# Kernel tuning notes

Hardware: AMD Instinct MI355X
Metric: run time of the kernel (lower is better)

The kernel has to match this reference:

```python
import jax, jax.numpy as jnp
import numpy as np

N_NODES = 100000
N_EDGES = 1600000
NFEAT, NHID, NCLASS = 256, 128, 40
N_CROSS = 20000


def setup_inputs() -> dict:
    key = jax.random.key(0)
    ks = jax.random.split(key, 16)
    s = 0.05
    return {
        "x": jax.random.normal(ks[0], (N_NODES, NFEAT), dtype=jnp.float32),
        "W0": jax.random.normal(ks[1], (NFEAT, NHID), dtype=jnp.float32) * s,
        "b0": jnp.zeros((NHID,), dtype=jnp.float32),
        "W1": jax.random.normal(ks[2], (NHID, NHID), dtype=jnp.float32) * s,
        "b1": jnp.zeros((NHID,), dtype=jnp.float32),
        "W2": jax.random.normal(ks[3], (NHID, NCLASS), dtype=jnp.float32) * s,
        "b2": jnp.zeros((NCLASS,), dtype=jnp.float32),
        "hist0": jax.random.normal(ks[4], (N_NODES, NHID), dtype=jnp.float32),
        "hist1": jax.random.normal(ks[5], (N_NODES, NHID), dtype=jnp.float32),
        "edge_src": jax.random.randint(ks[6], (N_EDGES,), 0, N_NODES, dtype=jnp.int32),
        "edge_dst": jax.random.randint(ks[7], (N_EDGES,), 0, N_NODES, dtype=jnp.int32),
        "idx_data0": jax.random.randint(ks[8], (N_CROSS,), 0, N_NODES, dtype=jnp.int32),
        "idx_com0": jax.random.randint(ks[9], (N_CROSS,), 0, N_NODES, dtype=jnp.int32),
        "idx_data1": jax.random.randint(ks[10], (N_CROSS,), 0, N_NODES, dtype=jnp.int32),
        "idx_com1": jax.random.randint(ks[11], (N_CROSS,), 0, N_NODES, dtype=jnp.int32),
    }


def reference(x, W0, b0, W1, b1, W2, b2, hist0, hist1,
              edge_src, edge_dst, idx_data0, idx_com0, idx_data1, idx_com1):
    N = x.shape[0]
    # GCN normalization with self-loops: A_hat = D^-1/2 (A + I) D^-1/2
    loops = jnp.arange(N, dtype=edge_src.dtype)
    src = jnp.concatenate([edge_src, loops])
    dst = jnp.concatenate([edge_dst, loops])
    deg = jax.ops.segment_sum(jnp.ones_like(dst, dtype=x.dtype), dst, num_segments=N)
    dis = jax.lax.rsqrt(jnp.maximum(deg, 1.0))  # deg >= 1 due to self-loops
    norm = (dis[src] * dis[dst])[:, None]       # [E+N, 1]

    def conv(h, W, b):
        h = h @ W                                             # [N, out]
        msg = h[src] * norm                                   # [E+N, out]
        return jax.ops.segment_sum(msg, dst, num_segments=N) + b

    # layer 0 + history overwrite (dropout is identity in eval mode)
    h = jax.nn.relu(conv(x, W0, b0))
    h = h.at[idx_com0].set(hist0[idx_data0])
    # layer 1 + history overwrite
    h = jax.nn.relu(conv(h, W1, b1))
    h = h.at[idx_com1].set(hist1[idx_data1])
    # final layer + log_softmax
    out = conv(h, W2, b2)
    return jax.nn.log_softmax(out, axis=-1)
```

## Files before the change

### kernel.cpp

```cpp
#include <hip/hip_runtime.h>
#include <cmath>

#define NFEAT 256
#define NHID  128
#define NCLASS 40
#define MAXNB 800
#define CHUNK 8192


__global__ __launch_bounds__(256)
void P1_hist(const int* __restrict__ dst, int* __restrict__ bh, int E, int NB){
  __shared__ int lh[MAXNB];
  for(int t = threadIdx.x; t < NB; t += 256) lh[t] = 0;
  __syncthreads();
  for(int i = blockIdx.x*256 + threadIdx.x; i < E; i += gridDim.x*256)
    atomicAdd(&lh[dst[i] >> 7], 1);
  __syncthreads();
  for(int t = threadIdx.x; t < NB; t += 256){
    int c = lh[t];
    if(c) atomicAdd(&bh[t], c);
  }
}

__global__ __launch_bounds__(1024)
void P2_scan(const int* __restrict__ bh, int* __restrict__ boff, int* __restrict__ bcur,
             int* __restrict__ off, int N, int E, int NB){
  __shared__ int sc[1024];
  int t = threadIdx.x;
  int v = (t < NB) ? bh[t] : 0;
  sc[t] = v; __syncthreads();
  for(int o = 1; o < 1024; o <<= 1){
    int a = sc[t] + ((t >= o) ? sc[t-o] : 0);
    __syncthreads();
    sc[t] = a;
    __syncthreads();
  }
  int ex = sc[t] - v;
  if(t < NB){ boff[t] = ex; bcur[t] = ex; }
  if(t == 0){ boff[NB] = E; off[N] = E; }
}

__global__ __launch_bounds__(256)
void P3_part(const int* __restrict__ src, const int* __restrict__ dst,
             int* __restrict__ bcur, int2* __restrict__ tmp, int E, int NB){
  __shared__ int dstS[CHUNK];
  __shared__ int lh[MAXNB];
  __shared__ int lcur[MAXNB];
  int base = blockIdx.x * CHUNK;
  int n = E - base; if(n > CHUNK) n = CHUNK;
  for(int t = threadIdx.x; t < NB; t += 256){ lh[t] = 0; lcur[t] = 0; }
  __syncthreads();
  for(int j = threadIdx.x; j < n; j += 256){
    int d = dst[base + j];
    dstS[j] = d;
    atomicAdd(&lh[d >> 7], 1);
  }
  __syncthreads();
  for(int t = threadIdx.x; t < NB; t += 256){
    int c = lh[t];
    if(c) lh[t] = atomicAdd(&bcur[t], c);
  }
  __syncthreads();
  for(int j = threadIdx.x; j < n; j += 256){
    int d = dstS[j];
    int b = d >> 7;
    int p = lh[b] + atomicAdd(&lcur[b], 1);
    tmp[p] = make_int2(src[base + j], d);
  }
}

__global__ __launch_bounds__(256)
void P4_build(const int2* __restrict__ tmp, const int* __restrict__ boff,
              int* __restrict__ off, float* __restrict__ dis,
              int* __restrict__ csr, int N){
  __shared__ int2 eS[3072];
  __shared__ int cnt[128], sc[128], cur[128];
  int b = blockIdx.x;
  int s = boff[b], e = boff[b+1];
  int ne = e - s;
  int n0 = b * 128;
  if(threadIdx.x < 128){ cnt[threadIdx.x] = 0; cur[threadIdx.x] = 0; }
  __syncthreads();
  bool fits = (ne <= 3072);
  for(int i = threadIdx.x; i < ne; i += 256){
    int2 p = tmp[s + i];
    if(fits) eS[i] = p;
    atomicAdd(&cnt[p.y & 127], 1);
  }
  __syncthreads();
  if(threadIdx.x < 128) sc[threadIdx.x] = cnt[threadIdx.x];
  __syncthreads();
  for(int o = 1; o < 128; o <<= 1){
    int a = 0;
    if(threadIdx.x < 128) a = sc[threadIdx.x] + ((threadIdx.x >= o) ? sc[threadIdx.x - o] : 0);
    __syncthreads();
    if(threadIdx.x < 128) sc[threadIdx.x] = a;
    __syncthreads();
  }
  if(threadIdx.x < 128){
    int node = n0 + threadIdx.x;
    if(node < N){
      int c = cnt[threadIdx.x];
      off[node] = s + sc[threadIdx.x] - c;
      dis[node] = rsqrtf((float)(c + 1));
    }
  }
  __syncthreads();
  for(int i = threadIdx.x; i < ne; i += 256){
    int2 p = fits ? eS[i] : tmp[s + i];
    int l = p.y & 127;
    int pos = s + (sc[l] - cnt[l]) + atomicAdd(&cur[l], 1);
    csr[pos] = p.x;
  }
}


template<int K, int NOUT>
__global__ __launch_bounds__(256)
void gemm_scale(const float* __restrict__ A, const float* __restrict__ W,
                const float* __restrict__ dis, float* __restrict__ C, int M)
{
  constexpr int BM = 128, BN = 64, BK = 16;
  __shared__ float As[BK][BM + 4];
  __shared__ float Ws[BK][BN];
  const int tid = threadIdx.x;
  const int tr = tid & 15;
  const int tc = tid >> 4;
  const int m0 = blockIdx.x * BM;
  const int n0 = blockIdx.y * BN;

  float acc[8][4];
  #pragma unroll
  for(int i = 0; i < 8; i++)
    #pragma unroll
    for(int j = 0; j < 4; j++) acc[i][j] = 0.f;

  for(int k0 = 0; k0 < K; k0 += BK){
    #pragma unroll
    for(int j = 0; j < 2; j++){
      int idx = tid + j*256;
      int row = idx & 127;
      int kq  = idx >> 7;
      float4 v = {0.f,0.f,0.f,0.f};
      int grow = m0 + row;
      if(grow < M) v = *reinterpret_cast<const float4*>(&A[(size_t)grow*K + k0 + kq*4]);
      As[kq*4+0][row] = v.x; As[kq*4+1][row] = v.y;
      As[kq*4+2][row] = v.z; As[kq*4+3][row] = v.w;
    }
    {
      int row = tid >> 4;
      int cq  = tid & 15;
      int col = n0 + cq*4;
      float4 v = {0.f,0.f,0.f,0.f};
      if(col + 3 < NOUT) v = *reinterpret_cast<const float4*>(&W[(size_t)(k0+row)*NOUT + col]);
      *reinterpret_cast<float4*>(&Ws[row][cq*4]) = v;
    }
    __syncthreads();
    #pragma unroll
    for(int k = 0; k < BK; k++){
      float4 a0 = *reinterpret_cast<const float4*>(&As[k][tr*8]);
      float4 a1 = *reinterpret_cast<const float4*>(&As[k][tr*8 + 4]);
      float4 bv = *reinterpret_cast<const float4*>(&Ws[k][tc*4]);
      float a[8] = {a0.x,a0.y,a0.z,a0.w,a1.x,a1.y,a1.z,a1.w};
      float bb[4] = {bv.x,bv.y,bv.z,bv.w};
      #pragma unroll
      for(int i = 0; i < 8; i++)
        #pragma unroll
        for(int j = 0; j < 4; j++)
          acc[i][j] += a[i]*bb[j];
    }
    __syncthreads();
  }
  #pragma unroll
  for(int i = 0; i < 8; i++){
    int grow = m0 + tr*8 + i;
    if(grow >= M) continue;
    int col = n0 + tc*4;
    if(col >= NOUT) continue;
    float d = dis[grow];
    float4 v;
    v.x = acc[i][0]*d; v.y = acc[i][1]*d; v.z = acc[i][2]*d; v.w = acc[i][3]*d;
    *reinterpret_cast<float4*>(&C[(size_t)grow*NOUT + col]) = v;
  }
}


__global__ __launch_bounds__(256)
void agg_relu128(const float* __restrict__ T, const int* __restrict__ off,
                 const int* __restrict__ csr, const float* __restrict__ dis,
                 const float* __restrict__ bias, float* __restrict__ H, int N)
{
  int node = blockIdx.x*4 + (threadIdx.x >> 6);
  if(node >= N) return;
  int lane = threadIdx.x & 63;
  int half = lane >> 5;
  int sl = lane & 31;
  int s = off[node], e = off[node+1];
  const float4* T4 = (const float4*)T;
  float4 acc = {0.f,0.f,0.f,0.f};
  for(int i = s + half; i < e; i += 2){
    int u = csr[i];
    float4 v = T4[(size_t)u*32 + sl];
    acc.x += v.x; acc.y += v.y; acc.z += v.z; acc.w += v.w;
  }
  if(half == 0){
    float4 v = T4[(size_t)node*32 + sl];
    acc.x += v.x; acc.y += v.y; acc.z += v.z; acc.w += v.w;
  }
  acc.x += __shfl_down(acc.x, 32, 64);
  acc.y += __shfl_down(acc.y, 32, 64);
  acc.z += __shfl_down(acc.z, 32, 64);
  acc.w += __shfl_down(acc.w, 32, 64);
  if(lane < 32){
    float di = dis[node];
    float4 b = ((const float4*)bias)[sl];
    float4 o;
    o.x = fmaxf(di*acc.x + b.x, 0.f);
    o.y = fmaxf(di*acc.y + b.y, 0.f);
    o.z = fmaxf(di*acc.z + b.z, 0.f);
    o.w = fmaxf(di*acc.w + b.w, 0.f);
    ((float4*)H)[(size_t)node*32 + sl] = o;
  }
}

__global__ __launch_bounds__(256)
void agg_softmax40(const float* __restrict__ T, const int* __restrict__ off,
                   const int* __restrict__ csr, const float* __restrict__ dis,
                   const float* __restrict__ bias, float* __restrict__ OUT, int N)
{
  int node = blockIdx.x*4 + (threadIdx.x >> 6);
  if(node >= N) return;
  int lane = threadIdx.x & 63;
  int g  = lane / 20;
  int sl = lane - g*20;
  int s = off[node], e = off[node+1];
  const float2* T2 = (const float2*)T;
  float ax = 0.f, ay = 0.f;
  if(g < 3){
    for(int i = s + g; i < e; i += 3){
      int u = csr[i];
      float2 v = T2[(size_t)u*20 + sl];
      ax += v.x; ay += v.y;
    }
    if(g == 0){
      float2 v = T2[(size_t)node*20 + sl];
      ax += v.x; ay += v.y;
    }
  }
  ax += __shfl(ax, lane + 20, 64) + __shfl(ax, lane + 40, 64);
  ay += __shfl(ay, lane + 20, 64) + __shfl(ay, lane + 40, 64);
  float di = dis[node];
  float vx = -1e30f, vy = -1e30f;
  if(lane < 20){
    float2 b = ((const float2*)bias)[sl];
    vx = di*ax + b.x;
    vy = di*ay + b.y;
  }
  float m = fmaxf(vx, vy);
  #pragma unroll
  for(int o = 1; o < 32; o <<= 1) m = fmaxf(m, __shfl_xor(m, o, 32));
  float ex = (lane < 20) ? (expf(vx - m) + expf(vy - m)) : 0.f;
  float ssum = ex;
  #pragma unroll
  for(int o = 1; o < 32; o <<= 1) ssum += __shfl_xor(ssum, o, 32);
  float lse = m + logf(ssum);
  if(lane < 20){
    float2 o2; o2.x = vx - lse; o2.y = vy - lse;
    ((float2*)OUT)[(size_t)node*20 + sl] = o2;
  }
}


__global__ void k_stamp(const int* __restrict__ idx_com, int* __restrict__ stamp, int n){
  int j = blockIdx.x*256 + threadIdx.x;
  if(j < n) atomicMax(&stamp[idx_com[j]], j);
}

__global__ __launch_bounds__(256)
void k_overwrite(const int* __restrict__ idx_com, const int* __restrict__ idx_data,
                 const int* __restrict__ stamp, const float* __restrict__ hist,
                 float* __restrict__ H, int n)
{
  int j = blockIdx.x*4 + (threadIdx.x >> 6);
  if(j >= n) return;
  int lane = threadIdx.x & 63;
  int c = idx_com[j];
  if(stamp[c] != j) return;
  int d = idx_data[j];
  ((float2*)H)[(size_t)c*64 + lane] = ((const float2*)hist)[(size_t)d*64 + lane];
}


extern "C" void kernel_launch(void* const* d_in, const int* in_sizes, int n_in,
                              void* d_out, int out_size, void* d_ws, size_t ws_size,
                              hipStream_t stream)
{
  const float* x     = (const float*)d_in[0];
  const float* W0    = (const float*)d_in[1];
  const float* b0    = (const float*)d_in[2];
  const float* W1    = (const float*)d_in[3];
  const float* b1    = (const float*)d_in[4];
  const float* W2    = (const float*)d_in[5];
  const float* b2    = (const float*)d_in[6];
  const float* hist0 = (const float*)d_in[7];
  const float* hist1 = (const float*)d_in[8];
  const int* esrc = (const int*)d_in[9];
  const int* edst = (const int*)d_in[10];
  const int* idx_data0 = (const int*)d_in[11];
  const int* idx_com0  = (const int*)d_in[12];
  const int* idx_data1 = (const int*)d_in[13];
  const int* idx_com1  = (const int*)d_in[14];

  const int N  = in_sizes[0] / NFEAT;
  const int E  = in_sizes[9];
  const int NC = in_sizes[11];
  const int NB = (N + 127) / 128;

  char* p = (char*)d_ws;
  auto carve = [&](size_t bytes) -> void* {
    void* r = (void*)p;
    p += (bytes + 255) & ~(size_t)255;
    return r;
  };
  int*   bh    = (int*)  carve((size_t)NB*4);
  int*   boff  = (int*)  carve((size_t)(NB+1)*4);
  int*   bcur  = (int*)  carve((size_t)NB*4);
  int*   off   = (int*)  carve((size_t)(N+1)*4);
  int*   stamp = (int*)  carve((size_t)N*4);
  int*   csr   = (int*)  carve((size_t)E*4);
  float* dis   = (float*)carve((size_t)N*4);
  float* bufA  = (float*)carve((size_t)N*NHID*4);
  float* bufB  = (float*)carve((size_t)N*NHID*4);
  size_t cbytes = (size_t)N*NCLASS*4;
  size_t tbytes = (size_t)E*8;
  float* bufC  = (float*)carve(cbytes > tbytes ? cbytes : tbytes);
  int2*  tmp   = (int2*)bufC;

  hipMemsetAsync(bh, 0, (size_t)NB*4, stream);
  P1_hist<<<256, 256, 0, stream>>>(edst, bh, E, NB);
  P2_scan<<<1, 1024, 0, stream>>>(bh, boff, bcur, off, N, E, NB);
  P3_part<<<(E + CHUNK - 1)/CHUNK, 256, 0, stream>>>(esrc, edst, bcur, tmp, E, NB);
  P4_build<<<NB, 256, 0, stream>>>(tmp, boff, off, dis, csr, N);

  dim3 g0((N + 127)/128, 2);
  gemm_scale<NFEAT, NHID><<<g0, 256, 0, stream>>>(x, W0, dis, bufA, N);
  agg_relu128<<<(N+3)/4, 256, 0, stream>>>(bufA, off, csr, dis, b0, bufB, N);

  hipMemsetAsync(stamp, 0xFF, (size_t)N*4, stream);
  k_stamp<<<(NC+255)/256, 256, 0, stream>>>(idx_com0, stamp, NC);
  k_overwrite<<<(NC+3)/4, 256, 0, stream>>>(idx_com0, idx_data0, stamp, hist0, bufB, NC);

  dim3 g1((N + 127)/128, 2);
  gemm_scale<NHID, NHID><<<g1, 256, 0, stream>>>(bufB, W1, dis, bufA, N);
  agg_relu128<<<(N+3)/4, 256, 0, stream>>>(bufA, off, csr, dis, b1, bufB, N);

  hipMemsetAsync(stamp, 0xFF, (size_t)N*4, stream);
  k_stamp<<<(NC+255)/256, 256, 0, stream>>>(idx_com1, stamp, NC);
  k_overwrite<<<(NC+3)/4, 256, 0, stream>>>(idx_com1, idx_data1, stamp, hist1, bufB, NC);

  dim3 g2((N + 127)/128, 1);
  gemm_scale<NHID, NCLASS><<<g2, 256, 0, stream>>>(bufB, W2, dis, bufC, N);
  agg_softmax40<<<(N+3)/4, 256, 0, stream>>>(bufC, off, csr, dis, b2, (float*)d_out, N);
}
```

Baseline: 797.8 us.

## Use full-width 128x128 GEMM tile and unroll gather loops with multiple accumulators

Adds a GEMM kernel that computes all 128 output columns per block with an 8x8 register tile per thread. This halves the number of times the A matrix is read compared with two 64-column blocks. The neighbour-aggregation loops in both aggregation kernels are unrolled with independent accumulators, so several gathers are in flight at once and memory latency is hidden. The cost is higher register pressure in the GEMM, which may reduce occupancy.

```diff
diff --git a/kernel.cpp b/kernel.cpp
--- a/kernel.cpp
+++ b/kernel.cpp
@@ -114,6 +114,75 @@
   }
 }
 
+
+template<int K>
+__global__ __launch_bounds__(256)
+void gemm128_scale(const float* __restrict__ A, const float* __restrict__ W,
+                   const float* __restrict__ dis, float* __restrict__ C, int M)
+{
+  constexpr int BM = 128, BK = 16;
+  __shared__ float As[BK][BM + 4];
+  __shared__ float Ws[BK][128 + 4];
+  const int tid = threadIdx.x;
+  const int tr = tid >> 4;
+  const int tc = tid & 15;
+  const int m0 = blockIdx.x * BM;
+
+  float acc[8][8];
+  #pragma unroll
+  for(int i = 0; i < 8; i++)
+    #pragma unroll
+    for(int j = 0; j < 8; j++) acc[i][j] = 0.f;
+
+  for(int k0 = 0; k0 < K; k0 += BK){
+    #pragma unroll
+    for(int j = 0; j < 2; j++){
+      int idx = tid + j*256;
+      int row = idx & 127;
+      int kq  = idx >> 7;
+      float4 v = {0.f,0.f,0.f,0.f};
+      int gr = m0 + row;
+      if(gr < M) v = *reinterpret_cast<const float4*>(&A[(size_t)gr*K + k0 + kq*4]);
+      As[kq*4+0][row] = v.x; As[kq*4+1][row] = v.y;
+      As[kq*4+2][row] = v.z; As[kq*4+3][row] = v.w;
+    }
+    #pragma unroll
+    for(int j = 0; j < 2; j++){
+      int idx = tid + j*256;
+      int row = idx >> 5;
+      int cq  = idx & 31;
+      float4 v = *reinterpret_cast<const float4*>(&W[(size_t)(k0+row)*128 + cq*4]);
+      *reinterpret_cast<float4*>(&Ws[row][cq*4]) = v;
+    }
+    __syncthreads();
+    #pragma unroll
+    for(int k = 0; k < BK; k++){
+      float4 a0 = *reinterpret_cast<const float4*>(&As[k][tr*4]);
+      float4 a1 = *reinterpret_cast<const float4*>(&As[k][64 + tr*4]);
+      float4 b0 = *reinterpret_cast<const float4*>(&Ws[k][tc*4]);
+      float4 b1 = *reinterpret_cast<const float4*>(&Ws[k][64 + tc*4]);
+      float a[8] = {a0.x,a0.y,a0.z,a0.w, a1.x,a1.y,a1.z,a1.w};
+      float b[8] = {b0.x,b0.y,b0.z,b0.w, b1.x,b1.y,b1.z,b1.w};
+      #pragma unroll
+      for(int i = 0; i < 8; i++)
+        #pragma unroll
+        for(int j = 0; j < 8; j++)
+          acc[i][j] += a[i]*b[j];
+    }
+    __syncthreads();
+  }
+  #pragma unroll
+  for(int i = 0; i < 8; i++){
+    int gr = m0 + ((i < 4) ? (tr*4 + i) : (64 + tr*4 + (i - 4)));
+    if(gr >= M) continue;
+    float d = dis[gr];
+    float4 v0, v1;
+    v0.x = acc[i][0]*d; v0.y = acc[i][1]*d; v0.z = acc[i][2]*d; v0.w = acc[i][3]*d;
+    v1.x = acc[i][4]*d; v1.y = acc[i][5]*d; v1.z = acc[i][6]*d; v1.w = acc[i][7]*d;
+    *reinterpret_cast<float4*>(&C[(size_t)gr*128 + tc*4]) = v0;
+    *reinterpret_cast<float4*>(&C[(size_t)gr*128 + 64 + tc*4]) = v1;
+  }
+}
 
 template<int K, int NOUT>
 __global__ __launch_bounds__(256)
@@ -197,16 +266,33 @@
   int sl = lane & 31;
   int s = off[node], e = off[node+1];
   const float4* T4 = (const float4*)T;
-  float4 acc = {0.f,0.f,0.f,0.f};
-  for(int i = s + half; i < e; i += 2){
+  float4 a0 = {0.f,0.f,0.f,0.f}, a1 = a0, a2 = a0, a3 = a0;
+  int i = s + half;
+  for(; i + 6 < e; i += 8){
+    int u0 = csr[i], u1 = csr[i+2], u2 = csr[i+4], u3 = csr[i+6];
+    float4 v0 = T4[(size_t)u0*32 + sl];
+    float4 v1 = T4[(size_t)u1*32 + sl];
+    float4 v2 = T4[(size_t)u2*32 + sl];
+    float4 v3 = T4[(size_t)u3*32 + sl];
+    a0.x += v0.x; a0.y += v0.y; a0.z += v0.z; a0.w += v0.w;
+    a1.x += v1.x; a1.y += v1.y; a1.z += v1.z; a1.w += v1.w;
+    a2.x += v2.x; a2.y += v2.y; a2.z += v2.z; a2.w += v2.w;
+    a3.x += v3.x; a3.y += v3.y; a3.z += v3.z; a3.w += v3.w;
+  }
+  for(; i < e; i += 2){
     int u = csr[i];
     float4 v = T4[(size_t)u*32 + sl];
-    acc.x += v.x; acc.y += v.y; acc.z += v.z; acc.w += v.w;
+    a0.x += v.x; a0.y += v.y; a0.z += v.z; a0.w += v.w;
   }
   if(half == 0){
     float4 v = T4[(size_t)node*32 + sl];
-    acc.x += v.x; acc.y += v.y; acc.z += v.z; acc.w += v.w;
-  }
+    a0.x += v.x; a0.y += v.y; a0.z += v.z; a0.w += v.w;
+  }
+  float4 acc;
+  acc.x = a0.x + a1.x + a2.x + a3.x;
+  acc.y = a0.y + a1.y + a2.y + a3.y;
+  acc.z = a0.z + a1.z + a2.z + a3.z;
+  acc.w = a0.w + a1.w + a2.w + a3.w;
   acc.x += __shfl_down(acc.x, 32, 64);
   acc.y += __shfl_down(acc.y, 32, 64);
   acc.z += __shfl_down(acc.z, 32, 64);
@@ -235,9 +321,19 @@
   int sl = lane - g*20;
   int s = off[node], e = off[node+1];
   const float2* T2 = (const float2*)T;
-  float ax = 0.f, ay = 0.f;
+  float ax = 0.f, ay = 0.f, bx = 0.f, by = 0.f, cx = 0.f, cy = 0.f;
   if(g < 3){
-    for(int i = s + g; i < e; i += 3){
+    int i = s + g;
+    for(; i + 6 < e; i += 9){
+      int u0 = csr[i], u1 = csr[i+3], u2 = csr[i+6];
+      float2 v0 = T2[(size_t)u0*20 + sl];
+      float2 v1 = T2[(size_t)u1*20 + sl];
+      float2 v2 = T2[(size_t)u2*20 + sl];
+      ax += v0.x; ay += v0.y;
+      bx += v1.x; by += v1.y;
+      cx += v2.x; cy += v2.y;
+    }
+    for(; i < e; i += 3){
       int u = csr[i];
       float2 v = T2[(size_t)u*20 + sl];
       ax += v.x; ay += v.y;
@@ -246,6 +342,7 @@
       float2 v = T2[(size_t)node*20 + sl];
       ax += v.x; ay += v.y;
     }
+    ax += bx + cx; ay += by + cy;
   }
   ax += __shfl(ax, lane + 20, 64) + __shfl(ax, lane + 40, 64);
   ay += __shfl(ay, lane + 20, 64) + __shfl(ay, lane + 40, 64);
@@ -342,23 +439,20 @@
   P3_part<<<(E + CHUNK - 1)/CHUNK, 256, 0, stream>>>(esrc, edst, bcur, tmp, E, NB);
   P4_build<<<NB, 256, 0, stream>>>(tmp, boff, off, dis, csr, N);
 
-  dim3 g0((N + 127)/128, 2);
-  gemm_scale<NFEAT, NHID><<<g0, 256, 0, stream>>>(x, W0, dis, bufA, N);
+  gemm128_scale<NFEAT><<<dim3((N + 127)/128, 1), 256, 0, stream>>>(x, W0, dis, bufA, N);
   agg_relu128<<<(N+3)/4, 256, 0, stream>>>(bufA, off, csr, dis, b0, bufB, N);
 
   hipMemsetAsync(stamp, 0xFF, (size_t)N*4, stream);
   k_stamp<<<(NC+255)/256, 256, 0, stream>>>(idx_com0, stamp, NC);
   k_overwrite<<<(NC+3)/4, 256, 0, stream>>>(idx_com0, idx_data0, stamp, hist0, bufB, NC);
 
-  dim3 g1((N + 127)/128, 2);
-  gemm_scale<NHID, NHID><<<g1, 256, 0, stream>>>(bufB, W1, dis, bufA, N);
+  gemm128_scale<NHID><<<dim3((N + 127)/128, 1), 256, 0, stream>>>(bufB, W1, dis, bufA, N);
   agg_relu128<<<(N+3)/4, 256, 0, stream>>>(bufA, off, csr, dis, b1, bufB, N);
 
   hipMemsetAsync(stamp, 0xFF, (size_t)N*4, stream);
   k_stamp<<<(NC+255)/256, 256, 0, stream>>>(idx_com1, stamp, NC);
   k_overwrite<<<(NC+3)/4, 256, 0, stream>>>(idx_com1, idx_data1, stamp, hist1, bufB, NC);
 
-  dim3 g2((N + 127)/128, 1);
-  gemm_scale<NHID, NCLASS><<<g2, 256, 0, stream>>>(bufB, W2, dis, bufC, N);
+  gemm_scale<NHID, NCLASS><<<dim3((N + 127)/128, 1), 256, 0, stream>>>(bufB, W2, dis, bufC, N);
   agg_softmax40<<<(N+3)/4, 256, 0, stream>>>(bufC, off, csr, dis, b2, (float*)d_out, N);
 }
```

Result: faster. 777.6 us (-2.5%).

## Use split-bf16 MFMA GEMMs and unroll neighbor aggregation loops

Applied to the files above, without the earlier changes.

Replaces the fp32 SIMT GEMMs with MFMA bf16 kernels. Each fp32 operand is split into high and low bf16 parts, and three MFMA products are summed to keep near-fp32 accuracy. Weights are pre-split and transposed by a small kernel on each call. The aggregation kernels also gain 4-way and 3-way unrolled gather loops with independent accumulators to expose more memory-level parallelism. This adds per-call weight-split launches and costs some precision versus true fp32.

```diff
diff --git a/kernel.cpp b/kernel.cpp
--- a/kernel.cpp
+++ b/kernel.cpp
@@ -6,6 +6,20 @@
 #define NCLASS 40
 #define MAXNB 800
 #define CHUNK 8192
+
+typedef __attribute__((ext_vector_type(8))) short bf16x8;
+typedef __attribute__((ext_vector_type(4))) float f32x4;
+
+__device__ __forceinline__ unsigned short f2bf(float f){
+  unsigned u = __float_as_uint(f);
+  u += 0x7FFFu + ((u >> 16) & 1u);
+  return (unsigned short)(u >> 16);
+}
+__device__ __forceinline__ void fsplit(float f, unsigned short &h, unsigned short &l){
+  h = f2bf(f);
+  float fh = __uint_as_float(((unsigned)h) << 16);
+  l = f2bf(f - fh);
+}
 
 
 __global__ __launch_bounds__(256)
@@ -115,72 +129,117 @@
 }
 
 
-template<int K, int NOUT>
-__global__ __launch_bounds__(256)
-void gemm_scale(const float* __restrict__ A, const float* __restrict__ W,
-                const float* __restrict__ dis, float* __restrict__ C, int M)
+__global__ void k_wsplit(const float* __restrict__ W, unsigned short* __restrict__ WTh,
+                         unsigned short* __restrict__ WTl, int K, int NOUT){
+  int n = blockIdx.x;
+  for(int k = threadIdx.x; k < K; k += blockDim.x){
+    float f = (n < NOUT) ? W[(size_t)k*NOUT + n] : 0.f;
+    unsigned short h, l;
+    fsplit(f, h, l);
+    WTh[(size_t)n*K + k] = h;
+    WTl[(size_t)n*K + k] = l;
+  }
+}
+
+
+template<int K, int BN>
+__global__ __launch_bounds__(256, 2)
+void gemm_mfma_scale(const float* __restrict__ A,
+                     const unsigned short* __restrict__ WTh,
+                     const unsigned short* __restrict__ WTl,
+                     const float* __restrict__ dis,
+                     float* __restrict__ C, int M, int NOUT)
 {
-  constexpr int BM = 128, BN = 64, BK = 16;
-  __shared__ float As[BK][BM + 4];
-  __shared__ float Ws[BK][BN];
-  const int tid = threadIdx.x;
-  const int tr = tid & 15;
-  const int tc = tid >> 4;
+  constexpr int BM = 128, BK = 32;
+  constexpr int WM = (BN == 128) ? 64 : 32;
+  constexpr int WN = 64;
+  constexpr int NWN = BN / WN;
+  constexpr int MF = WM / 16, NF = WN / 16;
+  __shared__ __align__(16) unsigned short AsH[BM][BK];
+  __shared__ __align__(16) unsigned short AsL[BM][BK];
+  __shared__ __align__(16) unsigned short WsH[BN][BK];
+  __shared__ __align__(16) unsigned short WsL[BN][BK];
+
+  const int tid  = threadIdx.x;
+  const int wave = tid >> 6;
+  const int lane = tid & 63;
+  const int wm = wave / NWN;
+  const int wn = wave % NWN;
   const int m0 = blockIdx.x * BM;
-  const int n0 = blockIdx.y * BN;
-
-  float acc[8][4];
+  const int lr = lane & 15;
+  const int lg = lane >> 4;
+
+  f32x4 acc[MF][NF];
   #pragma unroll
-  for(int i = 0; i < 8; i++)
-    #pragma unroll
-    for(int j = 0; j < 4; j++) acc[i][j] = 0.f;
+  for(int i = 0; i < MF; i++)
+    #pragma unroll
+    for(int j = 0; j < NF; j++)
+      acc[i][j] = (f32x4){0.f,0.f,0.f,0.f};
 
   for(int k0 = 0; k0 < K; k0 += BK){
     #pragma unroll
-    for(int j = 0; j < 2; j++){
-      int idx = tid + j*256;
-      int row = idx & 127;
-      int kq  = idx >> 7;
+    for(int j = 0; j < 4; j++){
+      int s   = tid + j*256;
+      int row = s >> 3;
+      int kq  = (s & 7) * 4;
       float4 v = {0.f,0.f,0.f,0.f};
-      int grow = m0 + row;
-      if(grow < M) v = *reinterpret_cast<const float4*>(&A[(size_t)grow*K + k0 + kq*4]);
-      As[kq*4+0][row] = v.x; As[kq*4+1][row] = v.y;
-      As[kq*4+2][row] = v.z; As[kq*4+3][row] = v.w;
-    }
-    {
-      int row = tid >> 4;
-      int cq  = tid & 15;
-      int col = n0 + cq*4;
-      float4 v = {0.f,0.f,0.f,0.f};
-      if(col + 3 < NOUT) v = *reinterpret_cast<const float4*>(&W[(size_t)(k0+row)*NOUT + col]);
-      *reinterpret_cast<float4*>(&Ws[row][cq*4]) = v;
-    }
-    __syncthreads();
-    #pragma unroll
-    for(int k = 0; k < BK; k++){
-      float4 a0 = *reinterpret_cast<const float4*>(&As[k][tr*8]);
-      float4 a1 = *reinterpret_cast<const float4*>(&As[k][tr*8 + 4]);
-      float4 bv = *reinterpret_cast<const float4*>(&Ws[k][tc*4]);
-      float a[8] = {a0.x,a0.y,a0.z,a0.w,a1.x,a1.y,a1.z,a1.w};
-      float bb[4] = {bv.x,bv.y,bv.z,bv.w};
+      if(m0 + row < M) v = *reinterpret_cast<const float4*>(&A[(size_t)(m0+row)*K + k0 + kq]);
+      ushort4 h, l;
+      fsplit(v.x, h.x, l.x); fsplit(v.y, h.y, l.y);
+      fsplit(v.z, h.z, l.z); fsplit(v.w, h.w, l.w);
+      *reinterpret_cast<ushort4*>(&AsH[row][kq]) = h;
+      *reinterpret_cast<ushort4*>(&AsL[row][kq]) = l;
+    }
+    constexpr int WSLOTS = BN * BK / 8;
+    #pragma unroll
+    for(int s = 0; s < WSLOTS; s += 256){
+      int ss = s + tid;
+      int n  = ss >> 2;
+      int kq = (ss & 3) * 8;
+      *reinterpret_cast<uint4*>(&WsH[n][kq]) =
+          *reinterpret_cast<const uint4*>(&WTh[(size_t)n*K + k0 + kq]);
+      *reinterpret_cast<uint4*>(&WsL[n][kq]) =
+          *reinterpret_cast<const uint4*>(&WTl[(size_t)n*K + k0 + kq]);
+    }
+    __syncthreads();
+
+    bf16x8 ah[MF], al[MF], bh[NF], bl[NF];
+    #pragma unroll
+    for(int i = 0; i < MF; i++){
+      ah[i] = *reinterpret_cast<const bf16x8*>(&AsH[wm*WM + i*16 + lr][lg*8]);
+      al[i] = *reinterpret_cast<const bf16x8*>(&AsL[wm*WM + i*16 + lr][lg*8]);
+    }
+    #pragma unroll
+    for(int j = 0; j < NF; j++){
+      bh[j] = *reinterpret_cast<const bf16x8*>(&WsH[wn*WN + j*16 + lr][lg*8]);
+      bl[j] = *reinterpret_cast<const bf16x8*>(&WsL[wn*WN + j*16 + lr][lg*8]);
+    }
+    #pragma unroll
+    for(int i = 0; i < MF; i++)
       #pragma unroll
-      for(int i = 0; i < 8; i++)
-        #pragma unroll
-        for(int j = 0; j < 4; j++)
-          acc[i][j] += a[i]*bb[j];
-    }
-    __syncthreads();
-  }
+      for(int j = 0; j < NF; j++){
+        acc[i][j] = __builtin_amdgcn_mfma_f32_16x16x32_bf16(ah[i], bh[j], acc[i][j], 0, 0, 0);
+        acc[i][j] = __builtin_amdgcn_mfma_f32_16x16x32_bf16(ah[i], bl[j], acc[i][j], 0, 0, 0);
+        acc[i][j] = __builtin_amdgcn_mfma_f32_16x16x32_bf16(al[i], bh[j], acc[i][j], 0, 0, 0);
+      }
+    __syncthreads();
+  }
+
   #pragma unroll
-  for(int i = 0; i < 8; i++){
-    int grow = m0 + tr*8 + i;
-    if(grow >= M) continue;
-    int col = n0 + tc*4;
-    if(col >= NOUT) continue;
-    float d = dis[grow];
-    float4 v;
-    v.x = acc[i][0]*d; v.y = acc[i][1]*d; v.z = acc[i][2]*d; v.w = acc[i][3]*d;
-    *reinterpret_cast<float4*>(&C[(size_t)grow*NOUT + col]) = v;
+  for(int i = 0; i < MF; i++){
+    int rbase = m0 + wm*WM + i*16 + lg*4;
+    #pragma unroll
+    for(int r = 0; r < 4; r++){
+      int row = rbase + r;
+      if(row >= M) continue;
+      float d = dis[row];
+      #pragma unroll
+      for(int j = 0; j < NF; j++){
+        int col = wn*WN + j*16 + lr;
+        if(col < NOUT)
+          C[(size_t)row*NOUT + col] = acc[i][j][r] * d;
+      }
+    }
   }
 }
 
@@ -197,16 +256,33 @@
   int sl = lane & 31;
   int s = off[node], e = off[node+1];
   const float4* T4 = (const float4*)T;
-  float4 acc = {0.f,0.f,0.f,0.f};
-  for(int i = s + half; i < e; i += 2){
+  float4 a0 = {0.f,0.f,0.f,0.f}, a1 = a0, a2 = a0, a3 = a0;
+  int i = s + half;
+  for(; i + 6 < e; i += 8){
+    int u0 = csr[i], u1 = csr[i+2], u2 = csr[i+4], u3 = csr[i+6];
+    float4 v0 = T4[(size_t)u0*32 + sl];
+    float4 v1 = T4[(size_t)u1*32 + sl];
+    float4 v2 = T4[(size_t)u2*32 + sl];
+    float4 v3 = T4[(size_t)u3*32 + sl];
+    a0.x += v0.x; a0.y += v0.y; a0.z += v0.z; a0.w += v0.w;
+    a1.x += v1.x; a1.y += v1.y; a1.z += v1.z; a1.w += v1.w;
+    a2.x += v2.x; a2.y += v2.y; a2.z += v2.z; a2.w += v2.w;
+    a3.x += v3.x; a3.y += v3.y; a3.z += v3.z; a3.w += v3.w;
+  }
+  for(; i < e; i += 2){
     int u = csr[i];
     float4 v = T4[(size_t)u*32 + sl];
-    acc.x += v.x; acc.y += v.y; acc.z += v.z; acc.w += v.w;
+    a0.x += v.x; a0.y += v.y; a0.z += v.z; a0.w += v.w;
   }
   if(half == 0){
     float4 v = T4[(size_t)node*32 + sl];
-    acc.x += v.x; acc.y += v.y; acc.z += v.z; acc.w += v.w;
-  }
+    a0.x += v.x; a0.y += v.y; a0.z += v.z; a0.w += v.w;
+  }
+  float4 acc;
+  acc.x = a0.x + a1.x + a2.x + a3.x;
+  acc.y = a0.y + a1.y + a2.y + a3.y;
+  acc.z = a0.z + a1.z + a2.z + a3.z;
+  acc.w = a0.w + a1.w + a2.w + a3.w;
   acc.x += __shfl_down(acc.x, 32, 64);
   acc.y += __shfl_down(acc.y, 32, 64);
   acc.z += __shfl_down(acc.z, 32, 64);
@@ -235,9 +311,19 @@
   int sl = lane - g*20;
   int s = off[node], e = off[node+1];
   const float2* T2 = (const float2*)T;
-  float ax = 0.f, ay = 0.f;
+  float ax = 0.f, ay = 0.f, bx = 0.f, by = 0.f, cx = 0.f, cy = 0.f;
   if(g < 3){
-    for(int i = s + g; i < e; i += 3){
+    int i = s + g;
+    for(; i + 6 < e; i += 9){
+      int u0 = csr[i], u1 = csr[i+3], u2 = csr[i+6];
+      float2 v0 = T2[(size_t)u0*20 + sl];
+      float2 v1 = T2[(size_t)u1*20 + sl];
+      float2 v2 = T2[(size_t)u2*20 + sl];
+      ax += v0.x; ay += v0.y;
+      bx += v1.x; by += v1.y;
+      cx += v2.x; cy += v2.y;
+    }
+    for(; i < e; i += 3){
       int u = csr[i];
       float2 v = T2[(size_t)u*20 + sl];
       ax += v.x; ay += v.y;
@@ -246,6 +332,7 @@
       float2 v = T2[(size_t)node*20 + sl];
       ax += v.x; ay += v.y;
     }
+    ax += bx + cx; ay += by + cy;
   }
   ax += __shfl(ax, lane + 20, 64) + __shfl(ax, lane + 40, 64);
   ay += __shfl(ay, lane + 20, 64) + __shfl(ay, lane + 40, 64);
@@ -329,6 +416,12 @@
   int*   stamp = (int*)  carve((size_t)N*4);
   int*   csr   = (int*)  carve((size_t)E*4);
   float* dis   = (float*)carve((size_t)N*4);
+  unsigned short* w0h = (unsigned short*)carve((size_t)128*256*2);
+  unsigned short* w0l = (unsigned short*)carve((size_t)128*256*2);
+  unsigned short* w1h = (unsigned short*)carve((size_t)128*128*2);
+  unsigned short* w1l = (unsigned short*)carve((size_t)128*128*2);
+  unsigned short* w2h = (unsigned short*)carve((size_t)64*128*2);
+  unsigned short* w2l = (unsigned short*)carve((size_t)64*128*2);
   float* bufA  = (float*)carve((size_t)N*NHID*4);
   float* bufB  = (float*)carve((size_t)N*NHID*4);
   size_t cbytes = (size_t)N*NCLASS*4;
@@ -336,29 +429,30 @@
   float* bufC  = (float*)carve(cbytes > tbytes ? cbytes : tbytes);
   int2*  tmp   = (int2*)bufC;
 
+  k_wsplit<<<128, 256, 0, stream>>>(W0, w0h, w0l, NFEAT, NHID);
+  k_wsplit<<<128, 256, 0, stream>>>(W1, w1h, w1l, NHID, NHID);
+  k_wsplit<<< 64, 256, 0, stream>>>(W2, w2h, w2l, NHID, NCLASS);
+
   hipMemsetAsync(bh, 0, (size_t)NB*4, stream);
   P1_hist<<<256, 256, 0, stream>>>(edst, bh, E, NB);
   P2_scan<<<1, 1024, 0, stream>>>(bh, boff, bcur, off, N, E, NB);
   P3_part<<<(E + CHUNK - 1)/CHUNK, 256, 0, stream>>>(esrc, edst, bcur, tmp, E, NB);
   P4_build<<<NB, 256, 0, stream>>>(tmp, boff, off, dis, csr, N);
 
-  dim3 g0((N + 127)/128, 2);
-  gemm_scale<NFEAT, NHID><<<g0, 256, 0, stream>>>(x, W0, dis, bufA, N);
+  gemm_mfma_scale<NFEAT, 128><<<NB, 256, 0, stream>>>(x, w0h, w0l, dis, bufA, N, NHID);
   agg_relu128<<<(N+3)/4, 256, 0, stream>>>(bufA, off, csr, dis, b0, bufB, N);
 
   hipMemsetAsync(stamp, 0xFF, (size_t)N*4, stream);
   k_stamp<<<(NC+255)/256, 256, 0, stream>>>(idx_com0, stamp, NC);
   k_overwrite<<<(NC+3)/4, 256, 0, stream>>>(idx_com0, idx_data0, stamp, hist0, bufB, NC);
 
-  dim3 g1((N + 127)/128, 2);
-  gemm_scale<NHID, NHID><<<g1, 256, 0, stream>>>(bufB, W1, dis, bufA, N);
+  gemm_mfma_scale<NHID, 128><<<NB, 256, 0, stream>>>(bufB, w1h, w1l, dis, bufA, N, NHID);
   agg_relu128<<<(N+3)/4, 256, 0, stream>>>(bufA, off, csr, dis, b1, bufB, N);
 
   hipMemsetAsync(stamp, 0xFF, (size_t)N*4, stream);
   k_stamp<<<(NC+255)/256, 256, 0, stream>>>(idx_com1, stamp, NC);
   k_overwrite<<<(NC+3)/4, 256, 0, stream>>>(idx_com1, idx_data1, stamp, hist1, bufB, NC);
 
-  dim3 g2((N + 127)/128, 1);
-  gemm_scale<NHID, NCLASS><<<g2, 256, 0, stream>>>(bufB, W2, dis, bufC, N);
+  gemm_mfma_scale<NHID, 64><<<NB, 256, 0, stream>>>(bufB, w2h, w2l, dis, bufC, N, NCLASS);
   agg_softmax40<<<(N+3)/4, 256, 0, stream>>>(bufC, off, csr, dis, b2, (float*)d_out, N);
 }
```

Result: faster. 732.9 us (-8.1%).
